# Kernel tuning notes

Measured on AMD Instinct MI355X. Metric: run time of the kernel, lower is better.

Reference implementation:

```python
import jax, jax.numpy as jnp
import numpy as np

SQRT_DK = np.sqrt(512.0).astype(np.float32)


def setup_inputs() -> dict:
    key = jax.random.key(0)
    k1, k2, k3 = jax.random.split(key, 3)
    x = jax.random.normal(k1, (16, 2048, 512), dtype=jnp.float32)
    W1 = jax.random.normal(k2, (512, 10), dtype=jnp.float32) * 0.05
    W2 = jax.random.normal(k3, (10, 512), dtype=jnp.float32) * 0.05
    return {"x": x, "W1": W1, "W2": W2}


def reference(x, W1, W2):
    # x: [B, A, D]; low-rank bilinear scores: (x@W1) @ (W2@x^T) -> [B, A, A]
    B, A, D = x.shape
    left = jnp.einsum('bad,dr->bar', x, W1)          # [B, A, 10]
    right = jnp.einsum('rd,bcd->brc', W2, x)         # [B, 10, A]
    scores = jnp.einsum('bar,brc->bac', left, right)  # [B, A, A]
    attn = jax.nn.softmax(scores / SQRT_DK, axis=-1)
    out = jnp.einsum('bac,bcd->bad', attn, x)         # requires_value=True
    return out
```

## Files before the change

kernel.cpp:

```cpp
#include <hip/hip_runtime.h>
#include <cstdint>
#include <cstddef>


typedef float    f32x4 __attribute__((ext_vector_type(4)));
typedef _Float16 half8 __attribute__((ext_vector_type(8)));
typedef _Float16 half4 __attribute__((ext_vector_type(4)));
typedef _Float16 half2 __attribute__((ext_vector_type(2)));

#define B_  16
#define A_  2048
#define D_  512
#define KSCALE 0.06375872f

__device__ inline float fast_exp2(float v) {
#if __has_builtin(__builtin_amdgcn_exp2f)
    return __builtin_amdgcn_exp2f(v);
#else
    return __expf(v * 0.6931471805599453f);
#endif
}

__global__ __launch_bounds__(256) void kw_prep(const float* __restrict__ W1,
                                               const float* __restrict__ W2,
                                               _Float16* __restrict__ Wf) {
    int pi = blockIdx.x * 256 + threadIdx.x;
    int kt = pi >> 6, lane = pi & 63;
    int quad = lane >> 4, col = lane & 15;
    half8 h1, h2;
#pragma unroll
    for (int j = 0; j < 8; ++j) {
        int d = kt * 32 + quad * 8 + j;
        h1[j] = (col < 10) ? (_Float16)(W1[d * 10 + col] * KSCALE) : (_Float16)0.f;
        h2[j] = (col < 10) ? (_Float16)W2[col * 512 + d] : (_Float16)0.f;
    }
    *(half8*)(Wf + (size_t)pi * 16) = h1;
    *(half8*)(Wf + (size_t)pi * 16 + 8) = h2;
}

__global__ __launch_bounds__(256) void kt_transpose(const float* __restrict__ x,
                                                    _Float16* __restrict__ xT) {
    __shared__ float xs[128 * 64];
    int t = threadIdx.x, w = t >> 6;
    int bid = blockIdx.x;
    int b = bid >> 7, cg = (bid >> 3) & 15, dg = bid & 7;
    int c0 = cg << 7, d0 = dg << 6;
    const float* xb = x + ((size_t)(b * A_ + c0)) * D_ + d0;
#pragma unroll
    for (int it = 0; it < 8; ++it) {
        int slot = it * 256 + t;
        int c = slot >> 4, g = slot & 15;
        int gs = g ^ (c >> 3);
        const float* src = xb + (size_t)c * D_ + (gs << 2);
        float* dst = xs + (size_t)(it * 256 + w * 64) * 4;
        __builtin_amdgcn_global_load_lds((const __attribute__((address_space(1))) void*)src,
                                         (__attribute__((address_space(3))) void*)dst,
                                         16, 0, 0);
    }
    __syncthreads();
    _Float16* xTb = xT + ((size_t)b * D_ + d0) * A_ + c0;
#pragma unroll
    for (int p = 0; p < 4; ++p) {
        int dloc = p * 16 + (t >> 4);
        int c8 = (t & 15) << 3;
        int gd = dloc >> 2, e = dloc & 3;
        half8 h;
#pragma unroll
        for (int j = 0; j < 8; ++j) {
            int c = c8 + j;
            h[j] = (_Float16)xs[c * 64 + ((gd ^ (c >> 3)) << 2) + e];
        }
        *(half8*)(xTb + (size_t)dloc * A_ + c8) = h;
    }
}

__global__ __launch_bounds__(256) void kf_factors(const float* __restrict__ x,
                                                  const _Float16* __restrict__ Wf,
                                                  _Float16* __restrict__ left16,
                                                  _Float16* __restrict__ rightT16) {
    int t = threadIdx.x, lane = t & 63, w = t >> 6;
    int quad = lane >> 4, c16 = lane & 15;
    size_t arow0 = (size_t)blockIdx.x * 64 + (size_t)w * 16;
    const float* xa = x + (arow0 + c16) * D_;
    f32x4 accA = {0.f, 0.f, 0.f, 0.f}, accB = {0.f, 0.f, 0.f, 0.f};
#pragma unroll
    for (int kc = 0; kc < 16; ++kc) {
        float4 v0 = *(const float4*)(xa + kc * 32 + quad * 8);
        float4 v1 = *(const float4*)(xa + kc * 32 + quad * 8 + 4);
        half8 af;
        af[0] = (_Float16)v0.x; af[1] = (_Float16)v0.y; af[2] = (_Float16)v0.z; af[3] = (_Float16)v0.w;
        af[4] = (_Float16)v1.x; af[5] = (_Float16)v1.y; af[6] = (_Float16)v1.z; af[7] = (_Float16)v1.w;
        const half8* wf = (const half8*)(Wf + ((size_t)(kc * 64 + lane)) * 16);
        accA = __builtin_amdgcn_mfma_f32_16x16x32_f16(af, wf[0], accA, 0, 0, 0);
        accB = __builtin_amdgcn_mfma_f32_16x16x32_f16(af, wf[1], accB, 0, 0, 0);
    }
#pragma unroll
    for (int q = 0; q < 4; ++q) {
        size_t grow = arow0 + (size_t)quad * 4 + q;
        left16[grow * 16 + c16]   = (_Float16)accA[q];
        rightT16[grow * 16 + c16] = (_Float16)accB[q];
    }
}

__global__ __launch_bounds__(512, 4) void k3_attn(const _Float16* __restrict__ xT,
                                                  const _Float16* __restrict__ left16,
                                                  const _Float16* __restrict__ rightT16,
                                                  float* __restrict__ out) {
    __shared__ _Float16 XTl[2][256 * 32];
    __shared__ _Float16 Ps[2][128 * 40];
    __shared__ float rowsum[128];
    int t = threadIdx.x, lane = t & 63, w = t >> 6;
    int quad = lane >> 4, c16 = lane & 15;
    int bid = blockIdx.x;
    int combo = (bid & 7) | (((bid >> 7) & 3) << 3);
    int at = (bid >> 3) & 15;
    int b = combo >> 1, nb = combo & 1;
    int a0 = at << 7, n0 = nb << 8;
    int waveM = w & 1, waveN = w >> 1;

    half8 lf8 = (half8)(_Float16)0.f;
    if (quad < 2) {
        int arow = a0 + w * 16 + c16;
        lf8 = *(const half8*)(left16 + ((size_t)(b << 11) + arow) * 16 + quad * 8);
    }

    f32x4 acc[4][4];
#pragma unroll
    for (int mi = 0; mi < 4; ++mi)
#pragma unroll
        for (int ni = 0; ni < 4; ++ni) acc[mi][ni] = (f32x4){0.f, 0.f, 0.f, 0.f};
    float psum = 0.f;

    const _Float16* xTb = xT + ((size_t)b * D_ + n0) * A_;
    const _Float16* rTb = rightT16 + (size_t)(b << 11) * 16;

    int nloc0 = w * 32 + (lane >> 2);
    int kq = lane & 3;

    auto dma_tile = [&](int kt, int buf) {
        int c0 = kt << 5;
#pragma unroll
        for (int cc = 0; cc < 2; ++cc) {
            int nl = nloc0 + cc * 16;
            int kqs = kq ^ ((nl >> 1) & 3);
            const _Float16* src = xTb + (size_t)nl * A_ + c0 + kqs * 8;
            _Float16* dst = &XTl[buf][(w * 32 + cc * 16) * 32];
            __builtin_amdgcn_global_load_lds((const __attribute__((address_space(1))) void*)src,
                                             (__attribute__((address_space(3))) void*)dst,
                                             16, 0, 0);
        }
    };
    auto load_bfr = [&](int kt, half8* bfr) {
#pragma unroll
        for (int nh = 0; nh < 2; ++nh) {
            bfr[nh] = (half8)(_Float16)0.f;
            if (quad < 2) {
                int crow = (kt << 5) + nh * 16 + c16;
                bfr[nh] = *(const half8*)(rTb + (size_t)crow * 16 + quad * 8);
            }
        }
    };
    auto p_phase = [&](const half8* bfr, int buf) {
#pragma unroll
        for (int nh = 0; nh < 2; ++nh) {
            f32x4 z = {0.f, 0.f, 0.f, 0.f};
            f32x4 pc = __builtin_amdgcn_mfma_f32_16x16x32_f16(bfr[nh], lf8, z, 0, 0, 0);
            float e0 = fast_exp2(pc[0]), e1 = fast_exp2(pc[1]);
            float e2 = fast_exp2(pc[2]), e3 = fast_exp2(pc[3]);
            psum += (e0 + e1) + (e2 + e3);
            half4 pv;
            pv[0] = (_Float16)e0; pv[1] = (_Float16)e1;
            pv[2] = (_Float16)e2; pv[3] = (_Float16)e3;
            *(half4*)&Ps[buf][(w * 16 + c16) * 40 + nh * 16 + quad * 4] = pv;
        }
    };

    {
        half8 bfr0[2];
        dma_tile(0, 0);
        load_bfr(0, bfr0);
        p_phase(bfr0, 0);
    }

    for (int kt = 0; kt < 64; ++kt) {
        __syncthreads();
        int cb = kt & 1, nxt = kt + 1;
        half8 bfr[2];
        if (nxt < 64) {
            dma_tile(nxt, nxt & 1);
            load_bfr(nxt, bfr);
        }
        half8 bf[4];
#pragma unroll
        for (int ni = 0; ni < 4; ++ni) {
            int nr = waveN * 64 + ni * 16 + c16;
            bf[ni] = *(const half8*)&XTl[cb][nr * 32 + ((quad ^ ((nr >> 1) & 3)) << 3)];
        }
        __builtin_amdgcn_s_setprio(1);
#pragma unroll
        for (int mi = 0; mi < 4; ++mi) {
            half8 af = *(const half8*)&Ps[cb][(waveM * 64 + mi * 16 + c16) * 40 + quad * 8];
#pragma unroll
            for (int ni = 0; ni < 4; ++ni)
                acc[mi][ni] = __builtin_amdgcn_mfma_f32_16x16x32_f16(af, bf[ni], acc[mi][ni], 0, 0, 0);
        }
        __builtin_amdgcn_s_setprio(0);
        if (nxt < 64) p_phase(bfr, nxt & 1);
    }

    {
        float s = psum;
        s += __shfl_xor(s, 16);
        s += __shfl_xor(s, 32);
        if (quad == 0) rowsum[w * 16 + c16] = s;
    }
    __syncthreads();

    float* ob = out + ((size_t)b * A_ + a0) * D_ + n0;
#pragma unroll
    for (int mi = 0; mi < 4; ++mi) {
#pragma unroll
        for (int q = 0; q < 4; ++q) {
            int ar = waveM * 64 + mi * 16 + quad * 4 + q;
            float sc = 1.0f / rowsum[ar];
#pragma unroll
            for (int ni = 0; ni < 4; ++ni)
                ob[(size_t)ar * D_ + waveN * 64 + ni * 16 + c16] = acc[mi][ni][q] * sc;
        }
    }
}

extern "C" void kernel_launch(void* const* d_in, const int* in_sizes, int n_in,
                              void* d_out, int out_size, void* d_ws, size_t ws_size,
                              hipStream_t stream) {
    const float* x  = (const float*)d_in[0];
    const float* W1 = (const float*)d_in[1];
    const float* W2 = (const float*)d_in[2];
    float* out = (float*)d_out;
    char* ws = (char*)d_ws;
    _Float16* xT      = (_Float16*)ws;
    _Float16* left16  = (_Float16*)(ws + 33554432);
    _Float16* rightT16= (_Float16*)(ws + 34603008);
    _Float16* Wf      = (_Float16*)(ws + 35651584);

    kw_prep<<<4, 256, 0, stream>>>(W1, W2, Wf);
    kt_transpose<<<2048, 256, 0, stream>>>(x, xT);
    kf_factors<<<512, 256, 0, stream>>>(x, Wf, left16, rightT16);
    k3_attn<<<512, 512, 0, stream>>>(xT, left16, rightT16, out);
}
```

Measured before the change: 208.1 us.

## Cover full D=512 per attention block with 1024 threads, sharing P computation

The attention kernel now launches 256 blocks of 1024 threads, and each block computes all 512 output columns for a 128-row tile instead of splitting D across two blocks. This removes the duplicated score/exp (P) computation and the duplicated rightT loads between the two D-halves. The P work is split so each wave computes one 16-column half, and row sums are reduced across two partial buffers. The cost is fewer blocks (256, close to the CU count), a larger shared-memory footprint, and heavier block-wide syncs, which may reduce occupancy and latency hiding.

Result: no change. 212.0 us (+1.9%).

```diff
diff --git a/kernel.cpp b/kernel.cpp
--- a/kernel.cpp
+++ b/kernel.cpp
@@ -102,25 +102,25 @@
     }
 }
 
-__global__ __launch_bounds__(512, 4) void k3_attn(const _Float16* __restrict__ xT,
-                                                  const _Float16* __restrict__ left16,
-                                                  const _Float16* __restrict__ rightT16,
-                                                  float* __restrict__ out) {
-    __shared__ _Float16 XTl[2][256 * 32];
+__global__ __launch_bounds__(1024, 4) void k3_attn(const _Float16* __restrict__ xT,
+                                                   const _Float16* __restrict__ left16,
+                                                   const _Float16* __restrict__ rightT16,
+                                                   float* __restrict__ out) {
+    __shared__ _Float16 XTl[2][512 * 32];
     __shared__ _Float16 Ps[2][128 * 40];
-    __shared__ float rowsum[128];
+    __shared__ float red[2][128];
     int t = threadIdx.x, lane = t & 63, w = t >> 6;
     int quad = lane >> 4, c16 = lane & 15;
     int bid = blockIdx.x;
-    int combo = (bid & 7) | (((bid >> 7) & 3) << 3);
+    int b = (bid & 7) | ((bid >> 7) << 3);
     int at = (bid >> 3) & 15;
-    int b = combo >> 1, nb = combo & 1;
-    int a0 = at << 7, n0 = nb << 8;
+    int a0 = at << 7;
     int waveM = w & 1, waveN = w >> 1;
+    int wp = w & 7, nhh = w >> 3;
 
     half8 lf8 = (half8)(_Float16)0.f;
     if (quad < 2) {
-        int arow = a0 + w * 16 + c16;
+        int arow = a0 + wp * 16 + c16;
         lf8 = *(const half8*)(left16 + ((size_t)(b << 11) + arow) * 16 + quad * 8);
     }
 
@@ -131,7 +131,7 @@
         for (int ni = 0; ni < 4; ++ni) acc[mi][ni] = (f32x4){0.f, 0.f, 0.f, 0.f};
     float psum = 0.f;
 
-    const _Float16* xTb = xT + ((size_t)b * D_ + n0) * A_;
+    const _Float16* xTb = xT + (size_t)b * D_ * A_;
     const _Float16* rTb = rightT16 + (size_t)(b << 11) * 16;
 
     int nloc0 = w * 32 + (lane >> 2);
@@ -150,45 +150,39 @@
                                              16, 0, 0);
         }
     };
-    auto load_bfr = [&](int kt, half8* bfr) {
-#pragma unroll
-        for (int nh = 0; nh < 2; ++nh) {
-            bfr[nh] = (half8)(_Float16)0.f;
-            if (quad < 2) {
-                int crow = (kt << 5) + nh * 16 + c16;
-                bfr[nh] = *(const half8*)(rTb + (size_t)crow * 16 + quad * 8);
-            }
-        }
+    auto load_bfr = [&](int kt) {
+        half8 bfr = (half8)(_Float16)0.f;
+        if (quad < 2) {
+            int crow = (kt << 5) + nhh * 16 + c16;
+            bfr = *(const half8*)(rTb + (size_t)crow * 16 + quad * 8);
+        }
+        return bfr;
     };
-    auto p_phase = [&](const half8* bfr, int buf) {
-#pragma unroll
-        for (int nh = 0; nh < 2; ++nh) {
-            f32x4 z = {0.f, 0.f, 0.f, 0.f};
-            f32x4 pc = __builtin_amdgcn_mfma_f32_16x16x32_f16(bfr[nh], lf8, z, 0, 0, 0);
-            float e0 = fast_exp2(pc[0]), e1 = fast_exp2(pc[1]);
-            float e2 = fast_exp2(pc[2]), e3 = fast_exp2(pc[3]);
-            psum += (e0 + e1) + (e2 + e3);
-            half4 pv;
-            pv[0] = (_Float16)e0; pv[1] = (_Float16)e1;
-            pv[2] = (_Float16)e2; pv[3] = (_Float16)e3;
-            *(half4*)&Ps[buf][(w * 16 + c16) * 40 + nh * 16 + quad * 4] = pv;
-        }
+    auto p_phase = [&](half8 bfr, int buf) {
+        f32x4 z = {0.f, 0.f, 0.f, 0.f};
+        f32x4 pc = __builtin_amdgcn_mfma_f32_16x16x32_f16(bfr, lf8, z, 0, 0, 0);
+        float e0 = fast_exp2(pc[0]), e1 = fast_exp2(pc[1]);
+        float e2 = fast_exp2(pc[2]), e3 = fast_exp2(pc[3]);
+        psum += (e0 + e1) + (e2 + e3);
+        half4 pv;
+        pv[0] = (_Float16)e0; pv[1] = (_Float16)e1;
+        pv[2] = (_Float16)e2; pv[3] = (_Float16)e3;
+        *(half4*)&Ps[buf][(wp * 16 + c16) * 40 + nhh * 16 + quad * 4] = pv;
     };
 
     {
-        half8 bfr0[2];
         dma_tile(0, 0);
-        load_bfr(0, bfr0);
+        half8 bfr0 = load_bfr(0);
         p_phase(bfr0, 0);
     }
 
     for (int kt = 0; kt < 64; ++kt) {
         __syncthreads();
         int cb = kt & 1, nxt = kt + 1;
-        half8 bfr[2];
+        half8 bfr = (half8)(_Float16)0.f;
         if (nxt < 64) {
             dma_tile(nxt, nxt & 1);
-            load_bfr(nxt, bfr);
+            bfr = load_bfr(nxt);
         }
         half8 bf[4];
 #pragma unroll
@@ -212,17 +206,17 @@
         float s = psum;
         s += __shfl_xor(s, 16);
         s += __shfl_xor(s, 32);
-        if (quad == 0) rowsum[w * 16 + c16] = s;
+        if (quad == 0) red[nhh][wp * 16 + c16] = s;
     }
     __syncthreads();
 
-    float* ob = out + ((size_t)b * A_ + a0) * D_ + n0;
+    float* ob = out + ((size_t)b * A_ + a0) * D_;
 #pragma unroll
     for (int mi = 0; mi < 4; ++mi) {
 #pragma unroll
         for (int q = 0; q < 4; ++q) {
             int ar = waveM * 64 + mi * 16 + quad * 4 + q;
-            float sc = 1.0f / rowsum[ar];
+            float sc = 1.0f / (red[0][ar] + red[1][ar]);
 #pragma unroll
             for (int ni = 0; ni < 4; ++ni)
                 ob[(size_t)ar * D_ + waveN * 64 + ni * 16 + c16] = acc[mi][ni][q] * sc;
@@ -246,5 +240,5 @@
     kw_prep<<<4, 256, 0, stream>>>(W1, W2, Wf);
     kt_transpose<<<2048, 256, 0, stream>>>(x, xT);
     kf_factors<<<512, 256, 0, stream>>>(x, Wf, left16, rightT16);
-    k3_attn<<<512, 512, 0, stream>>>(xT, left16, rightT16, out);
-}
+    k3_attn<<<256, 1024, 0, stream>>>(xT, left16, rightT16, out);
+}
```

## Interleave next-tile score MFMA and exp with PV MFMAs using sched barriers

Applied to the files above, without the earlier changes.

Restructures the main loop so the next tile's score MFMAs are issued at the top of the iteration. Their exp2 conversions and P stores are then split across the four PV MFMA groups, with sched_barrier fences keeping that interleaving in place. The right-factor loads are prefetched two tiles ahead and the last iteration is peeled out of the loop. The goal is to hide the transcendental and LDS work behind matrix-core work instead of running them serially after the MFMAs. It costs more live registers and removes the s_setprio hints.

Measured after the change: 203.7 us, median of 2. 1.02x faster.

```diff
diff --git a/kernel.cpp b/kernel.cpp
--- a/kernel.cpp
+++ b/kernel.cpp
@@ -6,12 +6,13 @@
 typedef float    f32x4 __attribute__((ext_vector_type(4)));
 typedef _Float16 half8 __attribute__((ext_vector_type(8)));
 typedef _Float16 half4 __attribute__((ext_vector_type(4)));
-typedef _Float16 half2 __attribute__((ext_vector_type(2)));
 
 #define B_  16
 #define A_  2048
 #define D_  512
 #define KSCALE 0.06375872f
+
+#define SCHED_FENCE() __builtin_amdgcn_sched_barrier(0)
 
 __device__ inline float fast_exp2(float v) {
 #if __has_builtin(__builtin_amdgcn_exp2f)
@@ -136,6 +137,7 @@
 
     int nloc0 = w * 32 + (lane >> 2);
     int kq = lane & 3;
+    int psrow = (w * 16 + c16) * 40;
 
     auto dma_tile = [&](int kt, int buf) {
         int c0 = kt << 5;
@@ -160,35 +162,36 @@
             }
         }
     };
-    auto p_phase = [&](const half8* bfr, int buf) {
-#pragma unroll
-        for (int nh = 0; nh < 2; ++nh) {
-            f32x4 z = {0.f, 0.f, 0.f, 0.f};
-            f32x4 pc = __builtin_amdgcn_mfma_f32_16x16x32_f16(bfr[nh], lf8, z, 0, 0, 0);
-            float e0 = fast_exp2(pc[0]), e1 = fast_exp2(pc[1]);
-            float e2 = fast_exp2(pc[2]), e3 = fast_exp2(pc[3]);
-            psum += (e0 + e1) + (e2 + e3);
-            half4 pv;
-            pv[0] = (_Float16)e0; pv[1] = (_Float16)e1;
-            pv[2] = (_Float16)e2; pv[3] = (_Float16)e3;
-            *(half4*)&Ps[buf][(w * 16 + c16) * 40 + nh * 16 + quad * 4] = pv;
-        }
-    };
-
+
+    half8 bfr_cur[2], bfr_nxt[2];
+    load_bfr(0, bfr_cur);
+    dma_tile(0, 0);
     {
-        half8 bfr0[2];
-        dma_tile(0, 0);
-        load_bfr(0, bfr0);
-        p_phase(bfr0, 0);
-    }
-
-    for (int kt = 0; kt < 64; ++kt) {
+        f32x4 zz = {0.f, 0.f, 0.f, 0.f};
+        f32x4 p0 = __builtin_amdgcn_mfma_f32_16x16x32_f16(bfr_cur[0], lf8, zz, 0, 0, 0);
+        f32x4 p1 = __builtin_amdgcn_mfma_f32_16x16x32_f16(bfr_cur[1], lf8, zz, 0, 0, 0);
+        float e0 = fast_exp2(p0[0]), e1 = fast_exp2(p0[1]), e2 = fast_exp2(p0[2]), e3 = fast_exp2(p0[3]);
+        float f0 = fast_exp2(p1[0]), f1 = fast_exp2(p1[1]), f2 = fast_exp2(p1[2]), f3 = fast_exp2(p1[3]);
+        psum += (e0 + e1) + (e2 + e3) + (f0 + f1) + (f2 + f3);
+        half4 pv0, pv1;
+        pv0[0] = (_Float16)e0; pv0[1] = (_Float16)e1; pv0[2] = (_Float16)e2; pv0[3] = (_Float16)e3;
+        pv1[0] = (_Float16)f0; pv1[1] = (_Float16)f1; pv1[2] = (_Float16)f2; pv1[3] = (_Float16)f3;
+        *(half4*)&Ps[0][psrow + quad * 4] = pv0;
+        *(half4*)&Ps[0][psrow + 16 + quad * 4] = pv1;
+    }
+    load_bfr(1, bfr_cur);
+
+    for (int kt = 0; kt < 63; ++kt) {
         __syncthreads();
-        int cb = kt & 1, nxt = kt + 1;
-        half8 bfr[2];
-        if (nxt < 64) {
-            dma_tile(nxt, nxt & 1);
-            load_bfr(nxt, bfr);
+        int cb = kt & 1, nx = kt + 1;
+
+        f32x4 zz = {0.f, 0.f, 0.f, 0.f};
+        f32x4 pc0 = __builtin_amdgcn_mfma_f32_16x16x32_f16(bfr_cur[0], lf8, zz, 0, 0, 0);
+        f32x4 pc1 = __builtin_amdgcn_mfma_f32_16x16x32_f16(bfr_cur[1], lf8, zz, 0, 0, 0);
+        dma_tile(nx, nx & 1);
+        {
+            int ktn = (kt + 2 < 64) ? kt + 2 : 0;
+            load_bfr(ktn, bfr_nxt);
         }
         half8 bf[4];
 #pragma unroll
@@ -196,7 +199,55 @@
             int nr = waveN * 64 + ni * 16 + c16;
             bf[ni] = *(const half8*)&XTl[cb][nr * 32 + ((quad ^ ((nr >> 1) & 3)) << 3)];
         }
-        __builtin_amdgcn_s_setprio(1);
+        half8 af0 = *(const half8*)&Ps[cb][(waveM * 64 + c16) * 40 + quad * 8];
+        SCHED_FENCE();
+
+        half8 af1 = *(const half8*)&Ps[cb][(waveM * 64 + 16 + c16) * 40 + quad * 8];
+#pragma unroll
+        for (int ni = 0; ni < 4; ++ni)
+            acc[0][ni] = __builtin_amdgcn_mfma_f32_16x16x32_f16(af0, bf[ni], acc[0][ni], 0, 0, 0);
+        float e0 = fast_exp2(pc0[0]), e1 = fast_exp2(pc0[1]);
+        float e2 = fast_exp2(pc0[2]), e3 = fast_exp2(pc0[3]);
+        psum += (e0 + e1) + (e2 + e3);
+        half4 pv0;
+        pv0[0] = (_Float16)e0; pv0[1] = (_Float16)e1; pv0[2] = (_Float16)e2; pv0[3] = (_Float16)e3;
+        SCHED_FENCE();
+
+        half8 af2 = *(const half8*)&Ps[cb][(waveM * 64 + 32 + c16) * 40 + quad * 8];
+#pragma unroll
+        for (int ni = 0; ni < 4; ++ni)
+            acc[1][ni] = __builtin_amdgcn_mfma_f32_16x16x32_f16(af1, bf[ni], acc[1][ni], 0, 0, 0);
+        float f0 = fast_exp2(pc1[0]), f1 = fast_exp2(pc1[1]);
+        float f2 = fast_exp2(pc1[2]), f3 = fast_exp2(pc1[3]);
+        psum += (f0 + f1) + (f2 + f3);
+        half4 pv1;
+        pv1[0] = (_Float16)f0; pv1[1] = (_Float16)f1; pv1[2] = (_Float16)f2; pv1[3] = (_Float16)f3;
+        SCHED_FENCE();
+
+        half8 af3 = *(const half8*)&Ps[cb][(waveM * 64 + 48 + c16) * 40 + quad * 8];
+#pragma unroll
+        for (int ni = 0; ni < 4; ++ni)
+            acc[2][ni] = __builtin_amdgcn_mfma_f32_16x16x32_f16(af2, bf[ni], acc[2][ni], 0, 0, 0);
+        *(half4*)&Ps[nx & 1][psrow + quad * 4] = pv0;
+        SCHED_FENCE();
+
+#pragma unroll
+        for (int ni = 0; ni < 4; ++ni)
+            acc[3][ni] = __builtin_amdgcn_mfma_f32_16x16x32_f16(af3, bf[ni], acc[3][ni], 0, 0, 0);
+        *(half4*)&Ps[nx & 1][psrow + 16 + quad * 4] = pv1;
+        bfr_cur[0] = bfr_nxt[0];
+        bfr_cur[1] = bfr_nxt[1];
+    }
+
+    __syncthreads();
+    {
+        const int cb = 1;
+        half8 bf[4];
+#pragma unroll
+        for (int ni = 0; ni < 4; ++ni) {
+            int nr = waveN * 64 + ni * 16 + c16;
+            bf[ni] = *(const half8*)&XTl[cb][nr * 32 + ((quad ^ ((nr >> 1) & 3)) << 3)];
+        }
 #pragma unroll
         for (int mi = 0; mi < 4; ++mi) {
             half8 af = *(const half8*)&Ps[cb][(waveM * 64 + mi * 16 + c16) * 40 + quad * 8];
@@ -204,8 +255,6 @@
             for (int ni = 0; ni < 4; ++ni)
                 acc[mi][ni] = __builtin_amdgcn_mfma_f32_16x16x32_f16(af, bf[ni], acc[mi][ni], 0, 0, 0);
         }
-        __builtin_amdgcn_s_setprio(0);
-        if (nxt < 64) p_phase(bfr, nxt & 1);
     }
 
     {
```
